# Optimization experiments

Hardware: AMD Instinct MI355X
Metric: run time of the kernel (lower is better)

Reference implementation:

```python
import math
import jax, jax.numpy as jnp
import numpy as np

INPUT_DIM = 1024
HEADS = 16
SEQ = 4096
BATCH = 1
SCALE = math.sqrt(INPUT_DIM / HEADS)  # 8.0


def setup_inputs() -> dict:
    key = jax.random.key(0)
    ks = jax.random.split(key, 5)
    D = INPUT_DIM
    return {
        "x": jax.random.normal(ks[0], (BATCH, SEQ, D), dtype=jnp.float32),
        "w_qkv": jax.random.normal(ks[1], (3 * D, D), dtype=jnp.float32) * (1.0 / math.sqrt(D)),
        "b_qkv": jax.random.normal(ks[2], (3 * D,), dtype=jnp.float32) * 0.01,
        "w_out": jax.random.normal(ks[3], (D, D), dtype=jnp.float32) * (1.0 / math.sqrt(D)),
        "b_out": jax.random.normal(ks[4], (D,), dtype=jnp.float32) * 0.01,
    }


def reference(x, w_qkv, b_qkv, w_out, b_out):
    b, n, D = x.shape
    h = HEADS
    d = D // h
    # qkv projection: [b, n, 3D]
    qkv = x @ w_qkv.T + b_qkv
    # 'b n (c h d) -> b c h n d' with c=3 outermost
    qkv = qkv.reshape(b, n, 3, h, d).transpose(2, 0, 3, 1, 4)  # [3, b, h, n, d]
    q, k, v = qkv[0], qkv[1], qkv[2]
    q = q / SCALE
    attn = jnp.einsum('bhnd,bhmd->bhnm', q, k)  # [b, h, n, n]
    attn = jax.nn.softmax(attn, axis=-1)
    # dropout is identity in eval mode
    context = jnp.einsum('bhnm,bhmd->bhnd', attn, v)  # [b, h, n, d]
    context = context.transpose(0, 2, 1, 3).reshape(b, n, D)  # 'b h n d -> b n (h d)'
    return context @ w_out.T + b_out
```

## Files before the change

kernel.cpp:

```cpp
#include <hip/hip_runtime.h>

typedef unsigned short u16;
typedef unsigned int u32;
typedef __attribute__((ext_vector_type(8))) short short8;
typedef __attribute__((ext_vector_type(4))) float f32x4;

__device__ __forceinline__ u16 f2b(float f) {
  union { float f; unsigned u; } v; v.f = f;
  unsigned r = (v.u + 0x7FFFu + ((v.u >> 16) & 1u)) >> 16;
  return (u16)r;
}
__device__ __forceinline__ float b2f(u16 b) {
  union { unsigned u; float f; } v; v.u = ((unsigned)b) << 16;
  return v.f;
}
__device__ __forceinline__ u32 cvtpk(float a, float b) {
  u32 r;
  asm("v_cvt_pk_bf16_f32 %0, %1, %2" : "=v"(r) : "v"(a), "v"(b));
  return r;
}
__device__ __forceinline__ void p32swap(u32& a, u32& b) {
  asm("v_permlane32_swap_b32 %0, %1" : "+v"(a), "+v"(b));
}
__device__ __forceinline__ void p16swap(u32& a, u32& b) {
  asm("v_permlane16_swap_b32 %0, %1" : "+v"(a), "+v"(b));
}
__device__ __forceinline__ float ldf(const void* p, size_t i, int f32) {
  return f32 ? ((const float*)p)[i] : b2f(((const u16*)p)[i]);
}

__global__ __launch_bounds__(256) void detect_dtype(const u16* __restrict__ x,
                                                    int* __restrict__ flag) {
  __shared__ int cnt;
  if (threadIdx.x == 0) cnt = 0;
  __syncthreads();
  int local = 0;
  for (int p = threadIdx.x; p < 512; p += 256) {
    int e = (x[2 * p] >> 7) & 0xFF;
    if (e >= 0xC0) local++;
  }
  atomicAdd(&cnt, local);
  __syncthreads();
  if (threadIdx.x == 0) flag[0] = (cnt >= 16) ? 1 : 0;
}

__global__ __launch_bounds__(256) void convert_all(
    const void* __restrict__ px, const void* __restrict__ pwq,
    const void* __restrict__ pbq, const void* __restrict__ pwo,
    const void* __restrict__ pbo, u16* __restrict__ xb,
    u16* __restrict__ wqkvb, u16* __restrict__ bqkvb, u16* __restrict__ wob,
    u16* __restrict__ bob, const int* __restrict__ flag) {
  int i = blockIdx.x * 256 + threadIdx.x;
  const void* in; u16* out; size_t g;
  if (i < 524288)       { in = px;  out = xb;    g = (size_t)i; }
  else if (i < 917504)  { in = pwq; out = wqkvb; g = (size_t)(i - 524288); }
  else if (i < 917888)  { in = pbq; out = bqkvb; g = (size_t)(i - 917504); }
  else if (i < 1048960) { in = pwo; out = wob;   g = (size_t)(i - 917888); }
  else                  { in = pbo; out = bob;   g = (size_t)(i - 1048960); }
  size_t base = g * 8;
  if (flag[0]) {
    const float* p = (const float*)in + base;
    float4 v0 = *(const float4*)p, v1 = *(const float4*)(p + 4);
    union { short8 v; u16 e[8]; } t;
    t.e[0]=f2b(v0.x); t.e[1]=f2b(v0.y); t.e[2]=f2b(v0.z); t.e[3]=f2b(v0.w);
    t.e[4]=f2b(v1.x); t.e[5]=f2b(v1.y); t.e[6]=f2b(v1.z); t.e[7]=f2b(v1.w);
    *(short8*)(out + base) = t.v;
  } else {
    *(short8*)(out + base) = *(const short8*)((const u16*)in + base);
  }
}

__global__ __launch_bounds__(256) void transpose_v(const u16* __restrict__ qkv,
                                                   u16* __restrict__ Vt) {
  __shared__ u16 T[64 * 72];
  const int tid = threadIdx.x;
  const int h = blockIdx.y;
  const int s0 = blockIdx.x * 64;
  for (int r = 0; r < 2; ++r) {
    int cid = r * 256 + tid;
    int s = cid >> 3, c8 = cid & 7;
    union { short8 v; u16 u[8]; } uu;
    uu.v = *(const short8*)(qkv + (size_t)(s0 + s) * 3072 + 2048 + h * 64 + c8 * 8);
    for (int i = 0; i < 8; ++i) T[(c8 * 8 + i) * 72 + s] = uu.u[i];
  }
  __syncthreads();
  for (int r = 0; r < 2; ++r) {
    int cid = r * 256 + tid;
    int dd = cid >> 3, c8 = cid & 7;
    union { short8 v; u16 u[8]; } uu;
    for (int i = 0; i < 8; ++i) uu.u[i] = T[dd * 72 + c8 * 8 + i];
    *(short8*)(Vt + (size_t)(h * 64 + dd) * 4096 + s0 + c8 * 8) = uu.v;
  }
}

__global__ __launch_bounds__(256) void gemm_bt(const void* __restrict__ A,
                                               const void* __restrict__ B,
                                               const void* __restrict__ bias,
                                               void* __restrict__ C,
                                               int M, int N, int K,
                                               int lda, int ldb, int ldc,
                                               int aMay, int bMay, int outF32,
                                               const int* __restrict__ flag) {
  __shared__ __align__(16) u16 sm[128 * 132];
  u16* As = sm;
  u16* Bs = sm + 128 * 64;
  const int f = flag[0];
  const int a32 = aMay && f, b32 = bMay && f;
  const int tid = threadIdx.x;
  const int w = tid >> 6, lane = tid & 63;
  const int lq = lane & 15, qr = lane >> 4;
  const int m0 = blockIdx.y * 128, n0 = blockIdx.x * 128;
  const int wm = (w >> 1) * 64, wn = (w & 1) * 64;

  f32x4 acc[4][4];
  for (int i = 0; i < 4; i++)
    for (int j = 0; j < 4; j++) acc[i][j] = (f32x4){0.f, 0.f, 0.f, 0.f};
  float bv[4];
  for (int ns = 0; ns < 4; ++ns) bv[ns] = ldf(bias, n0 + wn + ns * 16 + lq, b32);

  const int rs = tid >> 3, cs = tid & 7;
  const u16* gA = (const u16*)A + (size_t)(m0 + rs) * lda + cs * 8;
  const u16* gB = (const u16*)B + (size_t)(n0 + rs) * ldb + cs * 8;
  u16* lA = As + ((tid & ~63) << 3);
  u16* lB = Bs + ((tid & ~63) << 3);

  for (int k0 = 0; k0 < K; k0 += 64) {
    if (!(a32 | b32)) {
      for (int r = 0; r < 4; ++r) {
        __builtin_amdgcn_global_load_lds(gA + (size_t)(r * 32) * lda + k0,
                                         lA + r * 2048, 16, 0, 0);
        __builtin_amdgcn_global_load_lds(gB + (size_t)(r * 32) * ldb + k0,
                                         lB + r * 2048, 16, 0, 0);
      }
    } else {
      for (int r = 0; r < 4; ++r) {
        int cid = r * 256 + tid;
        int row = cid >> 3, c = cid & 7;
        if (a32) {
          const float* p = (const float*)A + (size_t)(m0 + row) * lda + k0 + c * 8;
          float4 v0 = *(const float4*)p, v1 = *(const float4*)(p + 4);
          union { short8 v; u16 e[8]; } t;
          t.e[0]=f2b(v0.x); t.e[1]=f2b(v0.y); t.e[2]=f2b(v0.z); t.e[3]=f2b(v0.w);
          t.e[4]=f2b(v1.x); t.e[5]=f2b(v1.y); t.e[6]=f2b(v1.z); t.e[7]=f2b(v1.w);
          *(short8*)(As + row * 64 + c * 8) = t.v;
        } else {
          *(short8*)(As + row * 64 + c * 8) =
              *(const short8*)((const u16*)A + (size_t)(m0 + row) * lda + k0 + c * 8);
        }
        if (b32) {
          const float* p = (const float*)B + (size_t)(n0 + row) * ldb + k0 + c * 8;
          float4 v0 = *(const float4*)p, v1 = *(const float4*)(p + 4);
          union { short8 v; u16 e[8]; } t;
          t.e[0]=f2b(v0.x); t.e[1]=f2b(v0.y); t.e[2]=f2b(v0.z); t.e[3]=f2b(v0.w);
          t.e[4]=f2b(v1.x); t.e[5]=f2b(v1.y); t.e[6]=f2b(v1.z); t.e[7]=f2b(v1.w);
          *(short8*)(Bs + row * 64 + c * 8) = t.v;
        } else {
          *(short8*)(Bs + row * 64 + c * 8) =
              *(const short8*)((const u16*)B + (size_t)(n0 + row) * ldb + k0 + c * 8);
        }
      }
    }
    __syncthreads();
    for (int ks = 0; ks < 2; ++ks) {
      short8 af[4], bf[4];
      const int sw = ks * 4 + qr;
      for (int i = 0; i < 4; i++) {
        af[i] = *(const short8*)(As + (wm + i * 16 + lq) * 64 + sw * 8);
        bf[i] = *(const short8*)(Bs + (wn + i * 16 + lq) * 64 + sw * 8);
      }
      for (int mi = 0; mi < 4; mi++)
        for (int ni = 0; ni < 4; ni++)
          acc[mi][ni] = __builtin_amdgcn_mfma_f32_16x16x32_bf16(
              af[mi], bf[ni], acc[mi][ni], 0, 0, 0);
    }
    __syncthreads();
  }

  if (!outF32) {
    u16* SH = sm;
    for (int mi = 0; mi < 4; mi++)
      for (int ni = 0; ni < 4; ni++)
        for (int r = 0; r < 4; ++r)
          SH[(wm + mi * 16 + qr * 4 + r) * 132 + wn + ni * 16 + lq] =
              f2b(acc[mi][ni][r] + bv[ni]);
    __syncthreads();
    for (int it = 0; it < 8; ++it) {
      int idx = it * 256 + tid;
      int row = idx >> 4, c8 = idx & 15;
      *(short8*)((u16*)C + (size_t)(m0 + row) * ldc + n0 + c8 * 8) =
          *(const short8*)(SH + row * 132 + c8 * 8);
    }
  } else {
    float* SHf = (float*)sm;
    for (int half = 0; half < 2; ++half) {
      if (half) __syncthreads();
      if ((w >> 1) == half) {
        for (int mi = 0; mi < 4; mi++)
          for (int ni = 0; ni < 4; ni++)
            for (int r = 0; r < 4; ++r)
              SHf[(mi * 16 + qr * 4 + r) * 132 + wn + ni * 16 + lq] =
                  acc[mi][ni][r] + bv[ni];
      }
      __syncthreads();
      for (int it = 0; it < 8; ++it) {
        int idx = it * 256 + tid;
        int row = idx >> 5, c4 = idx & 31;
        *(float4*)((float*)C + (size_t)(m0 + half * 64 + row) * ldc + n0 + c4 * 4) =
            *(const float4*)(SHf + row * 132 + c4 * 4);
      }
    }
  }
}

__global__ __launch_bounds__(256) void attn_fused(const u16* __restrict__ qkv,
                                                  const u16* __restrict__ Vtg,
                                                  u16* __restrict__ ctx, int ldctx) {
  __shared__ u16 Ks[64 * 64];
  __shared__ u16 Vts[64 * 64];
  const int tid = threadIdx.x;
  const int w = tid >> 6, lane = tid & 63;
  const int lq = lane & 15, qr = lane >> 4;
  const int qb = blockIdx.x, h = blockIdx.y;
  const int qbase = qb * 128 + w * 32;
  const float cs = 0.18033688011112042f;

  short8 qf[2][2];
  for (int mi = 0; mi < 2; ++mi)
    for (int ks = 0; ks < 2; ++ks)
      qf[mi][ks] = *(const short8*)(qkv + (size_t)(qbase + mi * 16 + lq) * 3072 +
                                    h * 64 + ks * 32 + qr * 8);

  f32x4 o[2][4];
  for (int mi = 0; mi < 2; ++mi)
    for (int ds = 0; ds < 4; ++ds) o[mi][ds] = (f32x4){0.f, 0.f, 0.f, 0.f};
  float lrow[2] = {0.f, 0.f};

  const int c = tid & 7, r0 = tid >> 3;
  u16* dKA = Ks + r0 * 64 + ((c ^ (r0 & 7)) << 3);
  u16* dKB = dKA + 32 * 64;
  u16* dVA = Vts + r0 * 64 + ((c ^ (r0 & 7)) << 3);
  u16* dVB = dVA + 32 * 64;
  const u16* sKA = qkv + (size_t)r0 * 3072 + 1024 + h * 64 + c * 8;
  const u16* sKB = sKA + (size_t)32 * 3072;
  const u16* sVA = Vtg ? (Vtg + (size_t)(h * 64 + r0) * 4096 + c * 8) : nullptr;
  const u16* sVB = Vtg ? (sVA + (size_t)32 * 4096) : nullptr;
  const u16* sVfA = qkv + (size_t)r0 * 3072 + 2048 + h * 64 + c * 8;
  const u16* sVfB = sVfA + (size_t)32 * 3072;

  short8 rKA, rKB, rVA, rVB;
  union { short8 v; u16 e[8]; } ufA, ufB;
  rKA = *(const short8*)sKA; sKA += (size_t)64 * 3072;
  rKB = *(const short8*)sKB; sKB += (size_t)64 * 3072;
  if (Vtg) {
    rVA = *(const short8*)sVA; sVA += 64;
    rVB = *(const short8*)sVB; sVB += 64;
  } else {
    ufA.v = *(const short8*)sVfA; sVfA += (size_t)64 * 3072;
    ufB.v = *(const short8*)sVfB; sVfB += (size_t)64 * 3072;
  }

  for (int j0 = 0; j0 < 4096; j0 += 64) {
    __syncthreads();
    *(short8*)dKA = rKA;
    *(short8*)dKB = rKB;
    if (Vtg) {
      *(short8*)dVA = rVA;
      *(short8*)dVB = rVB;
    } else {
      {
        const int jc = r0 >> 3, jl = r0 & 7;
        for (int i = 0; i < 8; ++i)
          Vts[(c * 8 + i) * 64 + ((jc ^ i) << 3) + jl] = ufA.e[i];
      }
      {
        const int jc = (r0 + 32) >> 3, jl = r0 & 7;
        for (int i = 0; i < 8; ++i)
          Vts[(c * 8 + i) * 64 + ((jc ^ i) << 3) + jl] = ufB.e[i];
      }
    }
    __syncthreads();

    if (j0 + 64 < 4096) {
      rKA = *(const short8*)sKA; sKA += (size_t)64 * 3072;
      rKB = *(const short8*)sKB; sKB += (size_t)64 * 3072;
      if (Vtg) {
        rVA = *(const short8*)sVA; sVA += 64;
        rVB = *(const short8*)sVB; sVB += 64;
      } else {
        ufA.v = *(const short8*)sVfA; sVfA += (size_t)64 * 3072;
        ufB.v = *(const short8*)sVfB; sVfB += (size_t)64 * 3072;
      }
    }

    f32x4 s[2][4];
    for (int mi = 0; mi < 2; ++mi)
      for (int ns = 0; ns < 4; ++ns) s[mi][ns] = (f32x4){0.f, 0.f, 0.f, 0.f};
    for (int ks = 0; ks < 2; ++ks) {
      short8 kf[4];
      for (int ns = 0; ns < 4; ++ns) {
        int rk = ns * 16 + lq;
        kf[ns] = *(const short8*)(Ks + rk * 64 + (((ks * 4 + qr) ^ (lq & 7)) << 3));
      }
      __builtin_amdgcn_s_setprio(1);
      for (int mi = 0; mi < 2; ++mi)
        for (int ns = 0; ns < 4; ++ns)
          s[mi][ns] = __builtin_amdgcn_mfma_f32_16x16x32_bf16(
              kf[ns], qf[mi][ks], s[mi][ns], 0, 0, 0);
      __builtin_amdgcn_s_setprio(0);
    }

    short8 pf[2][2];
#pragma unroll
    for (int mi = 0; mi < 2; ++mi) {
      float lacc = 0.f;
      u32 X[4], Y[4];
#pragma unroll
      for (int ns = 0; ns < 4; ++ns) {
        float p0 = __builtin_amdgcn_exp2f(fmaf(s[mi][ns][0], cs, -12.0f));
        float p1 = __builtin_amdgcn_exp2f(fmaf(s[mi][ns][1], cs, -12.0f));
        float p2 = __builtin_amdgcn_exp2f(fmaf(s[mi][ns][2], cs, -12.0f));
        float p3 = __builtin_amdgcn_exp2f(fmaf(s[mi][ns][3], cs, -12.0f));
        lacc += (p0 + p1) + (p2 + p3);
        X[ns] = cvtpk(p0, p1);
        Y[ns] = cvtpk(p2, p3);
      }
      lrow[mi] += lacc;
#pragma unroll
      for (int ks = 0; ks < 2; ++ks) {
        u32 a0 = X[2 * ks], b0 = X[2 * ks + 1];
        u32 a1 = Y[2 * ks], b1 = Y[2 * ks + 1];
        p32swap(a0, b0); p16swap(a0, b0);
        p32swap(a1, b1); p16swap(a1, b1);
        union { u32 u[4]; short8 v; } t;
        t.u[0] = a0; t.u[1] = a1; t.u[2] = b0; t.u[3] = b1;
        pf[mi][ks] = t.v;
      }
    }

    for (int ks = 0; ks < 2; ++ks) {
      short8 vf[4];
      for (int ds = 0; ds < 4; ++ds) {
        int dv = ds * 16 + lq;
        vf[ds] = *(const short8*)(Vts + (size_t)dv * 64 +
                                  (((ks * 4 + qr) ^ (lq & 7)) << 3));
      }
      __builtin_amdgcn_s_setprio(1);
      for (int mi = 0; mi < 2; ++mi)
        for (int ds = 0; ds < 4; ++ds)
          o[mi][ds] = __builtin_amdgcn_mfma_f32_16x16x32_bf16(
              vf[ds], pf[mi][ks], o[mi][ds], 0, 0, 0);
      __builtin_amdgcn_s_setprio(0);
    }
  }

  for (int mi = 0; mi < 2; ++mi) {
    float l = lrow[mi];
    l += __shfl_xor(l, 16, 64);
    l += __shfl_xor(l, 32, 64);
    float linv = 1.f / fmaxf(l, 1e-30f);
    int row = qbase + mi * 16 + lq;
    u16* dst = ctx + (size_t)row * ldctx + h * 64 + qr * 4;
    for (int ds = 0; ds < 4; ++ds) {
      u32 lo = cvtpk(o[mi][ds][0] * linv, o[mi][ds][1] * linv);
      u32 hi = cvtpk(o[mi][ds][2] * linv, o[mi][ds][3] * linv);
      *(uint2*)(dst + ds * 16) = make_uint2(lo, hi);
    }
  }
}

extern "C" void kernel_launch(void* const* d_in, const int* in_sizes, int n_in,
                              void* d_out, int out_size, void* d_ws, size_t ws_size,
                              hipStream_t stream) {
  float* out = (float*)d_out;

  const void *px = nullptr, *pwq = nullptr, *pbq = nullptr, *pwo = nullptr, *pbo = nullptr;
  if (n_in == 5) {
    for (int i = 0; i < 5; ++i) {
      switch (in_sizes[i]) {
        case 4194304: px = d_in[i]; break;
        case 3145728: pwq = d_in[i]; break;
        case 3072:    pbq = d_in[i]; break;
        case 1048576: pwo = d_in[i]; break;
        case 1024:    pbo = d_in[i]; break;
        default: break;
      }
    }
  }
  if (!px || !pwq || !pbq || !pwo || !pbo) {
    px = d_in[0]; pwq = d_in[1]; pbq = d_in[2]; pwo = d_in[3]; pbo = d_in[4];
  }

  int* flag = (int*)d_ws;
  u16* qkv = (u16*)((char*)d_ws + 64);
  u16* ctx = qkv;

  const size_t nQKV = (size_t)4096 * 3072;
  const size_t nVt = (size_t)16 * 64 * 4096;
  const size_t nx = 4194304, nwq = 3145728, nwo = 1048576;
  u16* Vtg = qkv + nQKV;
  const size_t need_vt = 64 + (nQKV + nVt) * 2;
  const size_t need_full = need_vt + (nx + nwq + 4096 + nwo + 1024) * 2;

  detect_dtype<<<1, 256, 0, stream>>>((const u16*)px, flag);

  if (ws_size >= need_full) {
    u16* xb    = Vtg + nVt;
    u16* wqkvb = xb + nx;
    u16* bqkvb = wqkvb + nwq;
    u16* wob   = bqkvb + 4096;
    u16* bob   = wob + nwo;
    convert_all<<<4098, 256, 0, stream>>>(px, pwq, pbq, pwo, pbo,
                                          xb, wqkvb, bqkvb, wob, bob, flag);

    gemm_bt<<<dim3(24, 32), 256, 0, stream>>>(xb, wqkvb, bqkvb, qkv,
                                              4096, 3072, 1024, 1024, 1024, 3072,
                                              0, 0, 0, flag);
    transpose_v<<<dim3(64, 16), 256, 0, stream>>>(qkv, Vtg);
    attn_fused<<<dim3(32, 16), 256, 0, stream>>>(qkv, Vtg, ctx, 3072);
    gemm_bt<<<dim3(8, 32), 256, 0, stream>>>(ctx, wob, bob, out,
                                             4096, 1024, 1024, 3072, 1024, 1024,
                                             0, 0, 1, flag);
  } else if (ws_size >= need_vt) {
    gemm_bt<<<dim3(24, 32), 256, 0, stream>>>(px, pwq, pbq, qkv,
                                              4096, 3072, 1024, 1024, 1024, 3072,
                                              1, 1, 0, flag);
    transpose_v<<<dim3(64, 16), 256, 0, stream>>>(qkv, Vtg);
    attn_fused<<<dim3(32, 16), 256, 0, stream>>>(qkv, Vtg, ctx, 3072);
    gemm_bt<<<dim3(8, 32), 256, 0, stream>>>(ctx, pwo, pbo, out,
                                             4096, 1024, 1024, 3072, 1024, 1024,
                                             0, 1, 1, flag);
  } else {
    gemm_bt<<<dim3(24, 32), 256, 0, stream>>>(px, pwq, pbq, qkv,
                                              4096, 3072, 1024, 1024, 1024, 3072,
                                              1, 1, 0, flag);
    attn_fused<<<dim3(32, 16), 256, 0, stream>>>(qkv, (const u16*)nullptr, ctx, 3072);
    gemm_bt<<<dim3(8, 32), 256, 0, stream>>>(ctx, pwo, pbo, out,
                                             4096, 1024, 1024, 3072, 1024, 1024,
                                             0, 1, 1, flag);
  }
}
```

Baseline: 279.0 us.

## Fuse V transpose into QKV GEMM epilogue and dtype detect into convert

The V transpose kernel is removed. The QKV GEMM epilogue now also writes the transposed V tile from shared memory into the Vt buffer for blocks covering the V columns. Dtype detection moves inside every convert_all block, dropping the separate detect launch on the main path. A block-index swizzle spreads consecutive workgroups across groups of eight for better cache locality. This saves two launches and an extra pass over V, at the cost of strided shared-memory reads in the epilogue and redundant per-block detection work.

```diff
diff --git a/kernel.cpp b/kernel.cpp
--- a/kernel.cpp
+++ b/kernel.cpp
@@ -49,7 +49,22 @@
     const void* __restrict__ pbq, const void* __restrict__ pwo,
     const void* __restrict__ pbo, u16* __restrict__ xb,
     u16* __restrict__ wqkvb, u16* __restrict__ bqkvb, u16* __restrict__ wob,
-    u16* __restrict__ bob, const int* __restrict__ flag) {
+    u16* __restrict__ bob) {
+  __shared__ int sf;
+  if (threadIdx.x == 0) sf = 0;
+  __syncthreads();
+  {
+    const u16* xr = (const u16*)px;
+    int local = 0;
+    for (int p = threadIdx.x; p < 512; p += 256) {
+      int e = (xr[2 * p] >> 7) & 0xFF;
+      if (e >= 0xC0) local++;
+    }
+    atomicAdd(&sf, local);
+  }
+  __syncthreads();
+  const int isf32 = (sf >= 16);
+
   int i = blockIdx.x * 256 + threadIdx.x;
   const void* in; u16* out; size_t g;
   if (i < 524288)       { in = px;  out = xb;    g = (size_t)i; }
@@ -58,7 +73,7 @@
   else if (i < 1048960) { in = pwo; out = wob;   g = (size_t)(i - 917888); }
   else                  { in = pbo; out = bob;   g = (size_t)(i - 1048960); }
   size_t base = g * 8;
-  if (flag[0]) {
+  if (isf32) {
     const float* p = (const float*)in + base;
     float4 v0 = *(const float4*)p, v1 = *(const float4*)(p + 4);
     union { short8 v; u16 e[8]; } t;
@@ -70,33 +85,11 @@
   }
 }
 
-__global__ __launch_bounds__(256) void transpose_v(const u16* __restrict__ qkv,
-                                                   u16* __restrict__ Vt) {
-  __shared__ u16 T[64 * 72];
-  const int tid = threadIdx.x;
-  const int h = blockIdx.y;
-  const int s0 = blockIdx.x * 64;
-  for (int r = 0; r < 2; ++r) {
-    int cid = r * 256 + tid;
-    int s = cid >> 3, c8 = cid & 7;
-    union { short8 v; u16 u[8]; } uu;
-    uu.v = *(const short8*)(qkv + (size_t)(s0 + s) * 3072 + 2048 + h * 64 + c8 * 8);
-    for (int i = 0; i < 8; ++i) T[(c8 * 8 + i) * 72 + s] = uu.u[i];
-  }
-  __syncthreads();
-  for (int r = 0; r < 2; ++r) {
-    int cid = r * 256 + tid;
-    int dd = cid >> 3, c8 = cid & 7;
-    union { short8 v; u16 u[8]; } uu;
-    for (int i = 0; i < 8; ++i) uu.u[i] = T[dd * 72 + c8 * 8 + i];
-    *(short8*)(Vt + (size_t)(h * 64 + dd) * 4096 + s0 + c8 * 8) = uu.v;
-  }
-}
-
 __global__ __launch_bounds__(256) void gemm_bt(const void* __restrict__ A,
                                                const void* __restrict__ B,
                                                const void* __restrict__ bias,
                                                void* __restrict__ C,
+                                               u16* __restrict__ VtOut,
                                                int M, int N, int K,
                                                int lda, int ldb, int ldc,
                                                int aMay, int bMay, int outF32,
@@ -109,7 +102,19 @@
   const int tid = threadIdx.x;
   const int w = tid >> 6, lane = tid & 63;
   const int lq = lane & 15, qr = lane >> 4;
-  const int m0 = blockIdx.y * 128, n0 = blockIdx.x * 128;
+
+  int bx = blockIdx.x, by = blockIdx.y;
+  {
+    int nwg = gridDim.x * gridDim.y;
+    if ((nwg & 7) == 0) {
+      int bid = by * gridDim.x + bx;
+      int cpx = nwg >> 3;
+      int swz = (bid & 7) * cpx + (bid >> 3);
+      bx = swz % gridDim.x;
+      by = swz / gridDim.x;
+    }
+  }
+  const int m0 = by * 128, n0 = bx * 128;
   const int wm = (w >> 1) * 64, wn = (w & 1) * 64;
 
   f32x4 acc[4][4];
@@ -190,6 +195,15 @@
       *(short8*)((u16*)C + (size_t)(m0 + row) * ldc + n0 + c8 * 8) =
           *(const short8*)(SH + row * 132 + c8 * 8);
     }
+    if (VtOut && n0 >= 2048) {
+      for (int it = 0; it < 8; ++it) {
+        int idx = it * 256 + tid;
+        int col = idx >> 4, sc = idx & 15;
+        union { short8 v; u16 e[8]; } t;
+        for (int i = 0; i < 8; ++i) t.e[i] = SH[(sc * 8 + i) * 132 + col];
+        *(short8*)(VtOut + (size_t)(n0 - 2048 + col) * 4096 + m0 + sc * 8) = t.v;
+      }
+    }
   } else {
     float* SHf = (float*)sm;
     for (int half = 0; half < 2; ++half) {
@@ -268,14 +282,14 @@
       *(short8*)dVB = rVB;
     } else {
       {
-        const int jc = r0 >> 3, jl = r0 & 7;
+        const int jc = r0 >> 3;
         for (int i = 0; i < 8; ++i)
-          Vts[(c * 8 + i) * 64 + ((jc ^ i) << 3) + jl] = ufA.e[i];
+          Vts[(c * 8 + i) * 64 + ((jc ^ i) << 3) + (r0 & 7)] = ufA.e[i];
       }
       {
-        const int jc = (r0 + 32) >> 3, jl = r0 & 7;
+        const int jc = (r0 + 32) >> 3;
         for (int i = 0; i < 8; ++i)
-          Vts[(c * 8 + i) * 64 + ((jc ^ i) << 3) + jl] = ufB.e[i];
+          Vts[(c * 8 + i) * 64 + ((jc ^ i) << 3) + (r0 & 7)] = ufB.e[i];
       }
     }
     __syncthreads();
@@ -401,8 +415,6 @@
   const size_t need_vt = 64 + (nQKV + nVt) * 2;
   const size_t need_full = need_vt + (nx + nwq + 4096 + nwo + 1024) * 2;
 
-  detect_dtype<<<1, 256, 0, stream>>>((const u16*)px, flag);
-
   if (ws_size >= need_full) {
     u16* xb    = Vtg + nVt;
     u16* wqkvb = xb + nx;
@@ -410,31 +422,31 @@
     u16* wob   = bqkvb + 4096;
     u16* bob   = wob + nwo;
     convert_all<<<4098, 256, 0, stream>>>(px, pwq, pbq, pwo, pbo,
-                                          xb, wqkvb, bqkvb, wob, bob, flag);
-
-    gemm_bt<<<dim3(24, 32), 256, 0, stream>>>(xb, wqkvb, bqkvb, qkv,
+                                          xb, wqkvb, bqkvb, wob, bob);
+
+    gemm_bt<<<dim3(24, 32), 256, 0, stream>>>(xb, wqkvb, bqkvb, qkv, Vtg,
                                               4096, 3072, 1024, 1024, 1024, 3072,
                                               0, 0, 0, flag);
-    transpose_v<<<dim3(64, 16), 256, 0, stream>>>(qkv, Vtg);
     attn_fused<<<dim3(32, 16), 256, 0, stream>>>(qkv, Vtg, ctx, 3072);
-    gemm_bt<<<dim3(8, 32), 256, 0, stream>>>(ctx, wob, bob, out,
+    gemm_bt<<<dim3(8, 32), 256, 0, stream>>>(ctx, wob, bob, out, nullptr,
                                              4096, 1024, 1024, 3072, 1024, 1024,
                                              0, 0, 1, flag);
   } else if (ws_size >= need_vt) {
-    gemm_bt<<<dim3(24, 32), 256, 0, stream>>>(px, pwq, pbq, qkv,
+    detect_dtype<<<1, 256, 0, stream>>>((const u16*)px, flag);
+    gemm_bt<<<dim3(24, 32), 256, 0, stream>>>(px, pwq, pbq, qkv, Vtg,
                                               4096, 3072, 1024, 1024, 1024, 3072,
                                               1, 1, 0, flag);
-    transpose_v<<<dim3(64, 16), 256, 0, stream>>>(qkv, Vtg);
     attn_fused<<<dim3(32, 16), 256, 0, stream>>>(qkv, Vtg, ctx, 3072);
-    gemm_bt<<<dim3(8, 32), 256, 0, stream>>>(ctx, pwo, pbo, out,
+    gemm_bt<<<dim3(8, 32), 256, 0, stream>>>(ctx, pwo, pbo, out, nullptr,
                                              4096, 1024, 1024, 3072, 1024, 1024,
                                              0, 1, 1, flag);
   } else {
-    gemm_bt<<<dim3(24, 32), 256, 0, stream>>>(px, pwq, pbq, qkv,
+    detect_dtype<<<1, 256, 0, stream>>>((const u16*)px, flag);
+    gemm_bt<<<dim3(24, 32), 256, 0, stream>>>(px, pwq, pbq, qkv, nullptr,
                                               4096, 3072, 1024, 1024, 1024, 3072,
                                               1, 1, 0, flag);
     attn_fused<<<dim3(32, 16), 256, 0, stream>>>(qkv, (const u16*)nullptr, ctx, 3072);
-    gemm_bt<<<dim3(8, 32), 256, 0, stream>>>(ctx, pwo, pbo, out,
+    gemm_bt<<<dim3(8, 32), 256, 0, stream>>>(ctx, pwo, pbo, out, nullptr,
                                              4096, 1024, 1024, 3072, 1024, 1024,
                                              0, 1, 1, flag);
   }
```

After: 282.8 us. No clear change (+1.4%).
